# Performance work log

Measured on AMD Instinct MI355X. Metric: run time of the kernel, lower is better.

## Reference

```python
import jax, jax.numpy as jnp
import numpy as np

B, S, E = 32, 1024, 512   # batch, source length, encoder/decoder/attn dim
D, U = 512, 512


def setup_inputs() -> dict:
    key = jax.random.key(0)
    k1, k2, k3, k4, k5 = jax.random.split(key, 5)
    return {
        "outp_enc": jax.random.normal(k1, (B, S, E), dtype=jnp.float32),
        "hidden_dec": jax.random.normal(k2, (B, D), dtype=jnp.float32),
        "Wa": jax.random.normal(k3, (D, U), dtype=jnp.float32) * (1.0 / np.sqrt(D)),
        "Ua": jax.random.normal(k4, (E, U), dtype=jnp.float32) * (1.0 / np.sqrt(E)),
        "Va": jax.random.normal(k5, (U,), dtype=jnp.float32) * (1.0 / np.sqrt(U)),
    }


def reference(outp_enc, hidden_dec, Wa, Ua, Va):
    # Additive (Bahdanau) attention.
    # energies: tanh(Wa h_dec + Ua enc_s) -> [B, S, U]
    dec_proj = hidden_dec @ Wa                      # [B, U]
    enc_proj = jnp.einsum("bse,eu->bsu", outp_enc, Ua)  # [B, S, U]
    e = jnp.tanh(enc_proj + dec_proj[:, None, :])   # [B, S, U]
    scores = jnp.einsum("bsu,u->bs", e, Va)          # [B, S]
    alpha = jax.nn.softmax(scores, axis=-1)          # [B, S]
    context = jnp.einsum("bs,bse->be", alpha, outp_enc)  # [B, E]
    return context
```

## Files before the change

kernel.cpp:

```cpp
#include <hip/hip_runtime.h>
#include <cstdint>
#include <cstddef>

#define BB 32
#define SS 1024
#define EE 512
#define UU 512
#define DD 512

typedef unsigned short ushort_t;
typedef __attribute__((ext_vector_type(8))) short s16x8;
typedef __attribute__((ext_vector_type(8))) _Float16 h16x8;
typedef __attribute__((ext_vector_type(4))) float f32x4;

#define AS1(p) ((const __attribute__((address_space(1))) void*)(const void*)(p))
#define AS3(p) ((__attribute__((address_space(3))) void*)(void*)(p))

__device__ inline float fast_tanh(float x) {
    float ax = fminf(fabsf(x), 20.0f);
    float e2 = __expf(ax * 2.0f);
    float t  = 1.0f - __fdividef(2.0f, e2 + 1.0f);
    return (x < 0.0f) ? -t : t;
}

__global__ void prep_kernel(const float* __restrict__ Ua,
                            const float* __restrict__ hid,
                            const float* __restrict__ Wa,
                            ushort_t* __restrict__ UaSwz,
                            float* __restrict__ decp) {
    __shared__ float sm[256];
    int blk = blockIdx.x, t = threadIdx.x;
    if (blk < 128) {
        int g    = blk * 256 + t;
        int tile = g >> 10;
        int c    = g & 1023;
        int nt = tile >> 3, kt = tile & 7;
        int n = c >> 3, kp = c & 7;
        int ko = kp ^ (n & 7);
        int u  = nt * 128 + n;
        int e0 = kt * 64 + ko * 8;
        s16x8 v;
#pragma unroll
        for (int j = 0; j < 8; ++j) {
            _Float16 h = (_Float16)Ua[(size_t)(e0 + j) * UU + u];
            v[j] = (short)__builtin_bit_cast(unsigned short, h);
        }
        *(s16x8*)(UaSwz + (size_t)g * 8) = v;
    } else {
        int q2 = blk - 128;
        int b = q2 >> 3, q = q2 & 7;
        int uo = t & 63, ch = t >> 6;
        const float* h = hid + (size_t)b * DD;
        float a = 0.f;
        int d0 = ch * 128;
#pragma unroll 4
        for (int d = d0; d < d0 + 128; ++d)
            a = fmaf(h[d], Wa[(size_t)d * UU + q * 64 + uo], a);
        sm[t] = a;
        __syncthreads();
        if (t < 64) {
            float s = sm[t] + sm[64 + t] + sm[128 + t] + sm[192 + t];
            decp[(size_t)b * UU + q * 64 + t] = s;
        }
    }
}

__global__ __launch_bounds__(128, 1)
void scores_kernel(const float* __restrict__ enc,
                   const ushort_t* __restrict__ UaSwz,
                   const float* __restrict__ decp,
                   const float* __restrict__ Va,
                   float* __restrict__ scores) {
    __shared__ __align__(16) ushort_t lds_b[2][8192];
    __shared__ float lds_dv[1024];

    const int tid  = threadIdx.x;
    const int lane = tid & 63;
    const int wave = tid >> 6;
    const int bid  = blockIdx.x;
    const int b    = bid >> 5;
    const int s0   = (bid & 31) * 32;

#pragma unroll
    for (int j = 0; j < 4; ++j)
        lds_dv[j * 128 + tid] = decp[(size_t)b * UU + j * 128 + tid];
#pragma unroll
    for (int j = 0; j < 4; ++j)
        lds_dv[512 + j * 128 + tid] = Va[j * 128 + tid];

    const int nl  = lane & 15;
    const int kq  = lane >> 4;
    const int l7  = lane & 7;
    const int rb  = nl * 64;
    const int kp0 = ((0 + kq) ^ l7) * 8;
    const int kp1 = ((4 + kq) ^ l7) * 8;

    const float* A = enc + ((size_t)b * SS + s0 + wave * 16 + nl) * EE + kq * 8;
    h16x8 a[16];
#pragma unroll
    for (int ks = 0; ks < 16; ++ks) {
        f32x4 v0 = *(const f32x4*)(A + ks * 32);
        f32x4 v1 = *(const f32x4*)(A + ks * 32 + 4);
        h16x8 sh;
#pragma unroll
        for (int j = 0; j < 4; ++j) {
            sh[j]     = (_Float16)v0[j];
            sh[4 + j] = (_Float16)v1[j];
        }
        a[ks] = sh;
    }

#define STAGE(tile, buf)                                                        \
    {                                                                           \
        _Pragma("unroll")                                                       \
        for (int i = 0; i < 8; ++i) {                                           \
            __builtin_amdgcn_global_load_lds(                                   \
                AS1(UaSwz + (size_t)(tile) * 8192 +                             \
                    ((i * 128 + wave * 64 + lane) * 8)),                        \
                AS3(&lds_b[buf][(i * 128 + wave * 64) * 8]), 16, 0, 0);         \
        }                                                                       \
    }

    f32x4 sp = {0.f, 0.f, 0.f, 0.f};

    __syncthreads();
    STAGE(0, 0);
    asm volatile("s_waitcnt vmcnt(0)" ::: "memory");
    __builtin_amdgcn_s_barrier();

#pragma unroll
    for (int nt = 0; nt < 4; ++nt) {
        f32x4 acc[8];
#pragma unroll
        for (int nf = 0; nf < 8; ++nf) acc[nf] = f32x4{0.f, 0.f, 0.f, 0.f};

#pragma unroll
        for (int kt = 0; kt < 8; ++kt) {
            const int t8 = nt * 8 + kt;
            if (t8 < 31) STAGE(t8 + 1, (t8 + 1) & 1);

            const ushort_t* bp = lds_b[t8 & 1];
#pragma unroll
            for (int ks = 0; ks < 2; ++ks) {
                const int kpo = ks ? kp1 : kp0;
#pragma unroll
                for (int nf = 0; nf < 8; ++nf) {
                    h16x8 bh = *(const h16x8*)(bp + nf * 1024 + rb + kpo);
                    acc[nf] = __builtin_amdgcn_mfma_f32_16x16x32_f16(
                        a[kt * 2 + ks], bh, acc[nf], 0, 0, 0);
                }
            }
            asm volatile("s_waitcnt lgkmcnt(0)" ::: "memory");
            asm volatile("s_waitcnt vmcnt(0)" ::: "memory");
            __builtin_amdgcn_s_barrier();
        }

#pragma unroll
        for (int nf = 0; nf < 8; ++nf) {
            int n = nt * 128 + nf * 16 + nl;
            float dp = lds_dv[n];
            float va = lds_dv[512 + n];
#pragma unroll
            for (int r = 0; r < 4; ++r)
                sp[r] += fast_tanh(acc[nf][r] + dp) * va;
        }
    }

#pragma unroll
    for (int off = 1; off < 16; off <<= 1) {
#pragma unroll
        for (int r = 0; r < 4; ++r)
            sp[r] += __shfl_xor(sp[r], off, 64);
    }
    if (nl == 0) {
        float* o = scores + (size_t)b * SS + s0 + wave * 16 + kq * 4;
#pragma unroll
        for (int r = 0; r < 4; ++r) o[r] = sp[r];
    }
#undef STAGE
}

__global__ void context_partial(const float* __restrict__ enc,
                                const float* __restrict__ sc,
                                float* __restrict__ part) {
    __shared__ float red[8];
    __shared__ float al[64];
    int bid = blockIdx.x;
    int b = bid >> 4, scn = bid & 15;
    int t = threadIdx.x, lane = t & 63, wave = t >> 6;

    f32x4 v = *(const f32x4*)(sc + (size_t)b * SS + t * 4);

    float m = fmaxf(fmaxf(v[0], v[1]), fmaxf(v[2], v[3]));
#pragma unroll
    for (int off = 1; off < 64; off <<= 1) m = fmaxf(m, __shfl_xor(m, off, 64));
    if (lane == 0) red[wave] = m;
    __syncthreads();
    m = fmaxf(fmaxf(red[0], red[1]), fmaxf(red[2], red[3]));

    float e0 = __expf(v[0] - m), e1 = __expf(v[1] - m);
    float e2 = __expf(v[2] - m), e3 = __expf(v[3] - m);
    float s = e0 + e1 + e2 + e3;
#pragma unroll
    for (int off = 1; off < 64; off <<= 1) s += __shfl_xor(s, off, 64);
    if (lane == 0) red[4 + wave] = s;
    __syncthreads();
    s = red[4] + red[5] + red[6] + red[7];
    float inv = 1.0f / s;

    if (t >= scn * 16 && t < scn * 16 + 16) {
        int i0 = (t - scn * 16) * 4;
        al[i0 + 0] = e0 * inv; al[i0 + 1] = e1 * inv;
        al[i0 + 2] = e2 * inv; al[i0 + 3] = e3 * inv;
    }
    __syncthreads();

    const float* basep = enc + ((size_t)b * SS + scn * 64) * EE;
    float a0 = 0.f, a1 = 0.f;
#pragma unroll 4
    for (int si = 0; si < 64; ++si) {
        float w = al[si];
        a0 = fmaf(w, basep[(size_t)si * EE + t], a0);
        a1 = fmaf(w, basep[(size_t)si * EE + t + 256], a1);
    }
    float* pp = part + ((size_t)scn * BB + b) * EE;
    pp[t] = a0;
    pp[t + 256] = a1;
}

__global__ void context_reduce(const float* __restrict__ part,
                               float* __restrict__ out) {
    int g = blockIdx.x * 256 + threadIdx.x;
    float s = 0.f;
#pragma unroll
    for (int scn = 0; scn < 16; ++scn) s += part[(size_t)scn * BB * EE + g];
    out[g] = s;
}

extern "C" void kernel_launch(void* const* d_in, const int* in_sizes, int n_in,
                              void* d_out, int out_size, void* d_ws, size_t ws_size,
                              hipStream_t stream) {
    const float* enc = (const float*)d_in[0];
    const float* hid = (const float*)d_in[1];
    const float* Wa  = (const float*)d_in[2];
    const float* Ua  = (const float*)d_in[3];
    const float* Va  = (const float*)d_in[4];
    float* out = (float*)d_out;

    char* ws = (char*)d_ws;
    float*    decp   = (float*)(ws);
    float*    scores = (float*)(ws + 65536);
    float*    part   = (float*)(ws + 196608);
    ushort_t* UaSwz  = (ushort_t*)(ws + 1245184);

    prep_kernel<<<384, 256, 0, stream>>>(Ua, hid, Wa, UaSwz, decp);
    scores_kernel<<<1024, 128, 0, stream>>>(enc, UaSwz, decp, Va, scores);
    context_partial<<<512, 256, 0, stream>>>(enc, scores, part);
    context_reduce<<<64, 256, 0, stream>>>(part, out);
}
```

Before: 77.71 us.

## Split U across blocks, keep Ua slice resident in LDS, XCD-aware mapping

```diff
diff --git a/kernel.cpp b/kernel.cpp
--- a/kernel.cpp
+++ b/kernel.cpp
@@ -65,123 +65,107 @@
     }
 }
 
-__global__ __launch_bounds__(128, 1)
+__global__ __launch_bounds__(512)
 void scores_kernel(const float* __restrict__ enc,
                    const ushort_t* __restrict__ UaSwz,
                    const float* __restrict__ decp,
                    const float* __restrict__ Va,
-                   float* __restrict__ scores) {
-    __shared__ __align__(16) ushort_t lds_b[2][8192];
-    __shared__ float lds_dv[1024];
+                   float* __restrict__ scpart) {
+    __shared__ __align__(16) ushort_t lds_b[65536];
+    __shared__ float lds_dv[256];
 
     const int tid  = threadIdx.x;
     const int lane = tid & 63;
     const int wave = tid >> 6;
-    const int bid  = blockIdx.x;
-    const int b    = bid >> 5;
-    const int s0   = (bid & 31) * 32;
-
-#pragma unroll
-    for (int j = 0; j < 4; ++j)
-        lds_dv[j * 128 + tid] = decp[(size_t)b * UU + j * 128 + tid];
-#pragma unroll
-    for (int j = 0; j < 4; ++j)
-        lds_dv[512 + j * 128 + tid] = Va[j * 128 + tid];
-
-    const int nl  = lane & 15;
-    const int kq  = lane >> 4;
-    const int l7  = lane & 7;
-    const int rb  = nl * 64;
-    const int kp0 = ((0 + kq) ^ l7) * 8;
-    const int kp1 = ((4 + kq) ^ l7) * 8;
-
-    const float* A = enc + ((size_t)b * SS + s0 + wave * 16 + nl) * EE + kq * 8;
-    h16x8 a[16];
-#pragma unroll
-    for (int ks = 0; ks < 16; ++ks) {
-        f32x4 v0 = *(const f32x4*)(A + ks * 32);
-        f32x4 v1 = *(const f32x4*)(A + ks * 32 + 4);
-        h16x8 sh;
-#pragma unroll
-        for (int j = 0; j < 4; ++j) {
-            sh[j]     = (_Float16)v0[j];
-            sh[4 + j] = (_Float16)v1[j];
-        }
-        a[ks] = sh;
-    }
-
-#define STAGE(tile, buf)                                                        \
-    {                                                                           \
-        _Pragma("unroll")                                                       \
-        for (int i = 0; i < 8; ++i) {                                           \
-            __builtin_amdgcn_global_load_lds(                                   \
-                AS1(UaSwz + (size_t)(tile) * 8192 +                             \
-                    ((i * 128 + wave * 64 + lane) * 8)),                        \
-                AS3(&lds_b[buf][(i * 128 + wave * 64) * 8]), 16, 0, 0);         \
-        }                                                                       \
-    }
-
-    f32x4 sp = {0.f, 0.f, 0.f, 0.f};
-
-    __syncthreads();
-    STAGE(0, 0);
+    const int p     = blockIdx.x;
+    const int xcd   = p & 7;
+    const int i     = p >> 3;
+    const int slice = xcd * 8 + (i >> 2);
+    const int q     = i & 3;
+    const int b     = slice >> 1;
+    const int half  = slice & 1;
+
+    if (tid < 128)      lds_dv[tid]       = decp[(size_t)b * UU + q * 128 + tid];
+    else if (tid < 256) lds_dv[tid]       = Va[q * 128 + (tid - 128)];
+
+#pragma unroll
+    for (int j = 0; j < 16; ++j) {
+        __builtin_amdgcn_global_load_lds(
+            AS1(UaSwz + (size_t)q * 65536 + ((j * 512 + wave * 64 + lane) * 8)),
+            AS3(&lds_b[(j * 512 + wave * 64) * 8]), 16, 0, 0);
+    }
+
+    const int nl = lane & 15;
+    const int kq = lane >> 4;
+    const int l7 = lane & 7;
+    const int soff0 = nl * 64 + (((0 + kq) ^ l7) * 8);
+    const int soff1 = nl * 64 + (((4 + kq) ^ l7) * 8);
+
+    const float* Abase = enc + ((size_t)b * SS + half * 512 + wave * 64 + nl) * EE
+                             + kq * 8;
+
+    f32x4 acc[4][8];
+#pragma unroll
+    for (int m = 0; m < 4; ++m)
+#pragma unroll
+        for (int nf = 0; nf < 8; ++nf) acc[m][nf] = f32x4{0.f, 0.f, 0.f, 0.f};
+
     asm volatile("s_waitcnt vmcnt(0)" ::: "memory");
     __builtin_amdgcn_s_barrier();
 
 #pragma unroll
-    for (int nt = 0; nt < 4; ++nt) {
-        f32x4 acc[8];
-#pragma unroll
-        for (int nf = 0; nf < 8; ++nf) acc[nf] = f32x4{0.f, 0.f, 0.f, 0.f};
-
-#pragma unroll
-        for (int kt = 0; kt < 8; ++kt) {
-            const int t8 = nt * 8 + kt;
-            if (t8 < 31) STAGE(t8 + 1, (t8 + 1) & 1);
-
-            const ushort_t* bp = lds_b[t8 & 1];
-#pragma unroll
-            for (int ks = 0; ks < 2; ++ks) {
-                const int kpo = ks ? kp1 : kp0;
-#pragma unroll
-                for (int nf = 0; nf < 8; ++nf) {
-                    h16x8 bh = *(const h16x8*)(bp + nf * 1024 + rb + kpo);
-                    acc[nf] = __builtin_amdgcn_mfma_f32_16x16x32_f16(
-                        a[kt * 2 + ks], bh, acc[nf], 0, 0, 0);
-                }
+    for (int kt = 0; kt < 16; ++kt) {
+        h16x8 am[4];
+#pragma unroll
+        for (int m = 0; m < 4; ++m) {
+            f32x4 v0 = *(const f32x4*)(Abase + m * 16 * EE + kt * 32);
+            f32x4 v1 = *(const f32x4*)(Abase + m * 16 * EE + kt * 32 + 4);
+            h16x8 h;
+#pragma unroll
+            for (int jj = 0; jj < 4; ++jj) {
+                h[jj]     = (_Float16)v0[jj];
+                h[4 + jj] = (_Float16)v1[jj];
             }
-            asm volatile("s_waitcnt lgkmcnt(0)" ::: "memory");
-            asm volatile("s_waitcnt vmcnt(0)" ::: "memory");
-            __builtin_amdgcn_s_barrier();
-        }
-
+            am[m] = h;
+        }
+        const ushort_t* bp = lds_b + (kt >> 1) * 8192 + ((kt & 1) ? soff1 : soff0);
 #pragma unroll
         for (int nf = 0; nf < 8; ++nf) {
-            int n = nt * 128 + nf * 16 + nl;
-            float dp = lds_dv[n];
-            float va = lds_dv[512 + n];
+            h16x8 bh = *(const h16x8*)(bp + nf * 1024);
+            acc[0][nf] = __builtin_amdgcn_mfma_f32_16x16x32_f16(am[0], bh, acc[0][nf], 0, 0, 0);
+            acc[1][nf] = __builtin_amdgcn_mfma_f32_16x16x32_f16(am[1], bh, acc[1][nf], 0, 0, 0);
+            acc[2][nf] = __builtin_amdgcn_mfma_f32_16x16x32_f16(am[2], bh, acc[2][nf], 0, 0, 0);
+            acc[3][nf] = __builtin_amdgcn_mfma_f32_16x16x32_f16(am[3], bh, acc[3][nf], 0, 0, 0);
+        }
+    }
+
+#pragma unroll
+    for (int m = 0; m < 4; ++m) {
+        f32x4 sp = {0.f, 0.f, 0.f, 0.f};
+#pragma unroll
+        for (int nf = 0; nf < 8; ++nf) {
+            float dp = lds_dv[nf * 16 + nl];
+            float va = lds_dv[128 + nf * 16 + nl];
 #pragma unroll
             for (int r = 0; r < 4; ++r)
-                sp[r] += fast_tanh(acc[nf][r] + dp) * va;
-        }
-    }
-
-#pragma unroll
-    for (int off = 1; off < 16; off <<= 1) {
-#pragma unroll
-        for (int r = 0; r < 4; ++r)
-            sp[r] += __shfl_xor(sp[r], off, 64);
-    }
-    if (nl == 0) {
-        float* o = scores + (size_t)b * SS + s0 + wave * 16 + kq * 4;
-#pragma unroll
-        for (int r = 0; r < 4; ++r) o[r] = sp[r];
-    }
-#undef STAGE
+                sp[r] += fast_tanh(acc[m][nf][r] + dp) * va;
+        }
+#pragma unroll
+        for (int off = 1; off < 16; off <<= 1) {
+#pragma unroll
+            for (int r = 0; r < 4; ++r)
+                sp[r] += __shfl_xor(sp[r], off, 64);
+        }
+        if (nl == 0) {
+            float* o = scpart + ((size_t)q * BB + b) * SS
+                     + half * 512 + wave * 64 + m * 16 + kq * 4;
+            o[0] = sp[0]; o[1] = sp[1]; o[2] = sp[2]; o[3] = sp[3];
+        }
+    }
 }
 
 __global__ void context_partial(const float* __restrict__ enc,
-                                const float* __restrict__ sc,
+                                const float* __restrict__ scp,
                                 float* __restrict__ part) {
     __shared__ float red[8];
     __shared__ float al[64];
@@ -189,7 +173,12 @@
     int b = bid >> 4, scn = bid & 15;
     int t = threadIdx.x, lane = t & 63, wave = t >> 6;
 
-    f32x4 v = *(const f32x4*)(sc + (size_t)b * SS + t * 4);
+    f32x4 v = {0.f, 0.f, 0.f, 0.f};
+#pragma unroll
+    for (int q = 0; q < 4; ++q) {
+        f32x4 u = *(const f32x4*)(scp + (size_t)q * BB * SS + (size_t)b * SS + t * 4);
+        v[0] += u[0]; v[1] += u[1]; v[2] += u[2]; v[3] += u[3];
+    }
 
     float m = fmaxf(fmaxf(v[0], v[1]), fmaxf(v[2], v[3]));
 #pragma unroll
@@ -249,12 +238,12 @@
 
     char* ws = (char*)d_ws;
     float*    decp   = (float*)(ws);
-    float*    scores = (float*)(ws + 65536);
-    float*    part   = (float*)(ws + 196608);
-    ushort_t* UaSwz  = (ushort_t*)(ws + 1245184);
+    float*    scpart = (float*)(ws + 65536);
+    ushort_t* UaSwz  = (ushort_t*)(ws + 589824);
+    float*    part   = (float*)(ws + 589824);
 
     prep_kernel<<<384, 256, 0, stream>>>(Ua, hid, Wa, UaSwz, decp);
-    scores_kernel<<<1024, 128, 0, stream>>>(enc, UaSwz, decp, Va, scores);
-    context_partial<<<512, 256, 0, stream>>>(enc, scores, part);
+    scores_kernel<<<256, 512, 0, stream>>>(enc, UaSwz, decp, Va, scpart);
+    context_partial<<<512, 256, 0, stream>>>(enc, scpart, part);
     context_reduce<<<64, 256, 0, stream>>>(part, out);
 }
```

New measurement: 79.30 us. 1.02x slower.
